# Optimization experiments

Measured on AMD Instinct MI355X. Metric: run time of the kernel, lower is better.

Reference implementation:

```python
import jax, jax.numpy as jnp
import numpy as np

C = 256
CQK = C // 8


def setup_inputs() -> dict:
    key = jax.random.key(0)
    ks = jax.random.split(key, 8)
    B, H, W = 4, 64, 64
    x = jax.random.normal(ks[0], (B, C, H, W), dtype=jnp.float32)
    # 1x1 conv weights are plain [out_c, in_c] matrices + bias
    sq = 1.0 / np.sqrt(C)
    Wq = jax.random.uniform(ks[1], (CQK, C), jnp.float32, -sq, sq)
    bq = jax.random.uniform(ks[2], (CQK,), jnp.float32, -sq, sq)
    Wk = jax.random.uniform(ks[3], (CQK, C), jnp.float32, -sq, sq)
    bk = jax.random.uniform(ks[4], (CQK,), jnp.float32, -sq, sq)
    Wv = jax.random.uniform(ks[5], (C, C), jnp.float32, -sq, sq)
    bv = jax.random.uniform(ks[6], (C,), jnp.float32, -sq, sq)
    gamma = jnp.zeros((1,), dtype=jnp.float32)
    return {"x": x, "Wq": Wq, "bq": bq, "Wk": Wk, "bk": bk, "Wv": Wv, "bv": bv, "gamma": gamma}


def reference(x, Wq, bq, Wk, bk, Wv, bv, gamma):
    B, Cc, H, W = x.shape
    N = H * W
    xf = x.reshape(B, Cc, N)  # [B, C, N]
    # 1x1 convs == channel GEMMs
    q = jnp.einsum('dc,bcn->bdn', Wq, xf) + bq[None, :, None]  # [B, C/8, N]
    k = jnp.einsum('dc,bcn->bdn', Wk, xf) + bk[None, :, None]  # [B, C/8, N]
    v = jnp.einsum('dc,bcn->bdn', Wv, xf) + bv[None, :, None]  # [B, C, N]
    # attention[b, i, j] = softmax_j( q_i . k_j )  (no scaling, as in source)
    attn = jax.nn.softmax(jnp.einsum('bdn,bdm->bnm', q, k), axis=-1)  # [B, N, N]
    # out = value @ attention  (note: NOT attention^T, faithful to source)
    out = jnp.einsum('bcn,bnm->bcm', v, attn)  # [B, C, N]
    out = out.reshape(B, Cc, H, W)
    return gamma[0] * out + x
```

## Files before the change

kernel.cpp:

```cpp
#include <hip/hip_runtime.h>
#include <hip/hip_bf16.h>


#define NB 4
#define CC 256
#define NN 4096
#define L2E 1.44269504088896340f

typedef short  short4v  __attribute__((ext_vector_type(4)));
typedef short  short8v  __attribute__((ext_vector_type(8)));
typedef __bf16 bf16x8   __attribute__((ext_vector_type(8)));
typedef float  f32x4    __attribute__((ext_vector_type(4)));
typedef float  f32x16   __attribute__((ext_vector_type(16)));
typedef unsigned long u64x2 __attribute__((ext_vector_type(2)));
typedef unsigned int u32;

#define AS1 __attribute__((address_space(1)))
#define AS3 __attribute__((address_space(3)))

static __device__ __forceinline__ void gload16(const void* g, void* l) {
  __builtin_amdgcn_global_load_lds((const AS1 u32*)g, (AS3 u32*)l, 16, 0, 0);
}

static __device__ __forceinline__ unsigned short f2bf(float f) {
  union { __bf16 h; unsigned short u; } v; v.h = (__bf16)f; return v.u;
}
static __device__ __forceinline__ float bf2f(unsigned short u) {
  union { unsigned u; float f; } v; v.u = (u32)u << 16; return v.f;
}

union FragU { short8v s; bf16x8 b; unsigned u[4]; };

static __device__ __forceinline__ bf16x8 ld_frag(const unsigned short* p) {
  FragU u; u.s = *(const short8v*)p; return u.b;
}

static __device__ __forceinline__ f32x16 zero16() {
  f32x16 v;
#pragma unroll
  for (int i = 0; i < 16; ++i) v[i] = 0.0f;
  return v;
}

static __device__ __forceinline__ f32x16 mfma32(bf16x8 a, bf16x8 b, f32x16 c) {
  return __builtin_amdgcn_mfma_f32_32x32x16_bf16(a, b, c, 0, 0, 0);
}

__global__ __launch_bounds__(256) void k_wcvt(
    const float* __restrict__ Wq, const float* __restrict__ Wk,
    const float* __restrict__ Wv, unsigned short* __restrict__ Wb)
{
  const int i4 = blockIdx.x * 256 + threadIdx.x;
  const int e = i4 * 4;
  const int row = e >> 8, c = e & 255;
  const float* src = (row < 32) ? (Wq + row * 256 + c)
                   : (row < 64) ? (Wk + (row - 32) * 256 + c)
                                : (Wv + (row - 64) * 256 + c);
  f32x4 v = *(const f32x4*)src;
  short4v s;
#pragma unroll
  for (int j = 0; j < 4; ++j) s[j] = (short)f2bf(v[j]);
  *(short4v*)(Wb + e) = s;
}

__global__ __launch_bounds__(256) void k_proj(
    const float* __restrict__ x, const unsigned short* __restrict__ Wb,
    const float* __restrict__ bq, const float* __restrict__ bk,
    const float* __restrict__ bv,
    unsigned short* __restrict__ Qt, unsigned short* __restrict__ Kt,
    unsigned char* __restrict__ V8)
{
  __shared__ unsigned short xs[32][268];
  const int t = threadIdx.x;
  const int b = blockIdx.y;
  const int n0 = blockIdx.x * 32;
  const int w = t >> 6, l = t & 63, h = l >> 5, col = l & 31;

  const float* xb = x + (size_t)b * CC * NN;
  {
    const int c_off = t >> 3, nl = 4 * (t & 7);
#pragma unroll
    for (int c0 = 0; c0 < CC; c0 += 32) {
      int c = c0 + c_off;
      f32x4 v4 = *(const f32x4*)(xb + (size_t)c * NN + n0 + nl);
#pragma unroll
      for (int j = 0; j < 4; ++j) xs[nl + j][c] = f2bf(v4[j]);
    }
  }
  __syncthreads();

  for (int f = w; f < 10; f += 4) {
    const float* bsrc; int rowbase; int mode; int wrow;
    if (f == 0)      { bsrc = bq; rowbase = 0;            mode = 0; wrow = 0; }
    else if (f == 1) { bsrc = bk; rowbase = 0;            mode = 1; wrow = 32; }
    else             { bsrc = bv; rowbase = (f - 2) * 32; mode = 2; wrow = 64 + rowbase; }

    f32x16 acc0 = zero16();
    const unsigned short* wr = Wb + (size_t)(wrow + col) * 256 + 8 * h;

#pragma unroll
    for (int k0 = 0; k0 < CC; k0 += 16) {
      FragU a;
      a.s = *(const short8v*)(wr + k0);
      const unsigned short* p0 = &xs[col][k0 + 8 * h];
      FragU b0;
      short4v t0a = *(const short4v*)p0, t0b = *(const short4v*)(p0 + 4);
#pragma unroll
      for (int j = 0; j < 4; ++j) { b0.s[j] = t0a[j]; b0.s[4 + j] = t0b[j]; }
      acc0 = mfma32(a.b, b0.b, acc0);
    }

    const int n = n0 + col;
#pragma unroll
    for (int q = 0; q < 4; ++q) {
      f32x4 bias4 = *(const f32x4*)(bsrc + rowbase + 8 * q + 4 * h);
      float vals[4];
#pragma unroll
      for (int i = 0; i < 4; ++i) vals[i] = acc0[4 * q + i] + bias4[i];
      if (mode == 2) {
        const size_t tb = (((size_t)b * (NN >> 4) + (n >> 4)) * 2 + ((n >> 3) & 1)) * CC * 8
                          + (n & 7);
        u32 w01 = __builtin_amdgcn_cvt_pk_fp8_f32(vals[0], vals[1], 0, false);
        u32 w23 = __builtin_amdgcn_cvt_pk_fp8_f32(vals[2], vals[3], 0, false);
        const int cb0 = rowbase + 8 * q + 4 * h;
        V8[tb + (size_t)(cb0 + 0) * 8] = (unsigned char)(w01 & 0xff);
        V8[tb + (size_t)(cb0 + 1) * 8] = (unsigned char)((w01 >> 8) & 0xff);
        V8[tb + (size_t)(cb0 + 2) * 8] = (unsigned char)(w23 & 0xff);
        V8[tb + (size_t)(cb0 + 3) * 8] = (unsigned char)((w23 >> 8) & 0xff);
      } else {
        unsigned short* dst = (mode == 0) ? Qt : Kt;
        const float scale = (mode == 0) ? L2E : 1.0f;
        short4v s4;
#pragma unroll
        for (int i = 0; i < 4; ++i) s4[i] = (short)f2bf(vals[i] * scale);
        *(short4v*)(dst + ((size_t)b * NN + n) * 32 + 8 * q + 4 * h) = s4;
      }
    }
  }
}

__global__ __launch_bounds__(256) void k_rowstats(
    const unsigned short* __restrict__ Qt, const unsigned short* __restrict__ Kt,
    float* __restrict__ cbias)
{
  __shared__ float ssum[4][32];
  const int t = threadIdx.x;
  const int w = t >> 6, l = t & 63, h = l >> 5, col = l & 31;
  const int b = blockIdx.y;
  const int n0 = blockIdx.x * 32;
  const unsigned short* Qb = Qt + (size_t)b * NN * 32;
  const unsigned short* Kb = Kt + (size_t)b * NN * 32;

  bf16x8 bq0 = ld_frag(Qb + (size_t)(n0 + col) * 32 + 8 * h);
  bf16x8 bq1 = ld_frag(Qb + (size_t)(n0 + col) * 32 + 16 + 8 * h);

  float acc = 0.0f;
  const int mbase = w * (NN / 4);
#pragma unroll 2
  for (int mt = 0; mt < 32; ++mt) {
    const int m0 = mbase + mt * 32;
    bf16x8 ak0 = ld_frag(Kb + (size_t)(m0 + col) * 32 + 8 * h);
    bf16x8 ak1 = ld_frag(Kb + (size_t)(m0 + col) * 32 + 16 + 8 * h);
    f32x16 S = zero16();
    S = mfma32(ak0, bq0, S);
    S = mfma32(ak1, bq1, S);
    float p0 = 0.0f, p1 = 0.0f, p2 = 0.0f, p3 = 0.0f;
#pragma unroll
    for (int r = 0; r < 4; ++r) {
      p0 += __builtin_amdgcn_exp2f(S[r]);
      p1 += __builtin_amdgcn_exp2f(S[4 + r]);
      p2 += __builtin_amdgcn_exp2f(S[8 + r]);
      p3 += __builtin_amdgcn_exp2f(S[12 + r]);
    }
    acc += (p0 + p1) + (p2 + p3);
  }
  acc += __shfl_xor(acc, 32);

  if (l < 32) ssum[w][l] = acc;
  __syncthreads();

  if (t < 32) {
    float s = (ssum[0][t] + ssum[1][t]) + (ssum[2][t] + ssum[3][t]);
    cbias[(size_t)b * NN + n0 + t] = -__builtin_amdgcn_logf(s);
  }
}

__global__ __launch_bounds__(512) void k_attn_out(
    const unsigned short* __restrict__ Qt, const unsigned short* __restrict__ Kt,
    const unsigned char* __restrict__ V8,
    const float* __restrict__ cbias,
    unsigned short* __restrict__ pout,
    int nsplit, int nlen)
{
  __shared__ __align__(16) char qbuf[2][2][2048];
  __shared__ __align__(16) char vbuf[3][2][8192];
  __shared__ __align__(16) char ebuf[2][2][4096];

  const int wg = (int)blockIdx.x;
  const int chunk = (int)gridDim.x >> 3;
  const int id2 = (wg & 7) * chunk + (wg >> 3);
  const int per_b = 32 * nsplit;
  const int b = id2 / per_b;
  const int rem = id2 - b * per_b;
  const int ns = rem >> 5;
  const int m0 = (rem & 31) * 128;
  const int nbeg = ns * nlen;

  const int t = threadIdx.x;
  const int w = t >> 6, l = t & 63, h = l >> 5, col = l & 31;
  const int mfp = w & 3;
  const int ccons = (w & 3) * 64;

  const unsigned short* Kb = Kt + (size_t)b * NN * 32;
  const float* cb = cbias + (size_t)b * NN + nbeg;

  bf16x8 bk0 = ld_frag(Kb + (size_t)(m0 + 32 * mfp + col) * 32 + 8 * h);
  bf16x8 bk1 = ld_frag(Kb + (size_t)(m0 + 32 * mfp + col) * 32 + 16 + 8 * h);

  const int ll = l & 15;
  const size_t gqoff = (size_t)(((w & 1) * 16 + ll) * 64 + ((w >> 1) & 1) * 16
                                + (w >> 2) * 32);
  const char* qsrc = (const char*)Qt + ((size_t)b * NN + nbeg) * 64 + gqoff;
  const char* vsrc = (const char*)V8 + ((size_t)b * (NN >> 4) + (nbeg >> 4)) * 4096
                     + (size_t)t * 16;

  f32x16 acc[4][2];
#pragma unroll
  for (int mf = 0; mf < 4; ++mf)
#pragma unroll
    for (int cf = 0; cf < 2; ++cf) acc[mf][cf] = zero16();

  const int J = nlen >> 6;

  if (ll == l) {
    gload16(qsrc, &qbuf[0][0][w * 256]);
    gload16(qsrc + 2048, &qbuf[0][1][w * 256]);
  }
  gload16(vsrc, &vbuf[0][0][w * 1024]);
  gload16(vsrc + 8192, &vbuf[0][1][w * 1024]);
  __syncthreads();

  for (int j = 0; j <= J; ++j) {
    if (j + 1 < J) {
      const size_t qoff = (size_t)(2 * j + 2) * 2048;
      const size_t voff = (size_t)(2 * j + 2) * 8192;
      const int qs = (j + 1) & 1, vs = (j + 1) % 3;
      if (ll == l) {
        gload16(qsrc + qoff, &qbuf[qs][0][w * 256]);
        gload16(qsrc + qoff + 2048, &qbuf[qs][1][w * 256]);
      }
      gload16(vsrc + voff, &vbuf[vs][0][w * 1024]);
      gload16(vsrc + voff + 8192, &vbuf[vs][1][w * 1024]);
    }

    if (w < 4) {
      if (j < J) {
#pragma unroll
        for (int u = 0; u < 2; ++u) {
          const char* qb = &qbuf[j & 1][u][0];
          FragU fq0, fq1;
          fq0.s = *(const short8v*)(qb + l * 16);
          fq1.s = *(const short8v*)(qb + 1024 + l * 16);
          f32x16 S = zero16();
          S = mfma32(fq0.b, bk0, S);
          S = mfma32(fq1.b, bk1, S);

          float e[16];
          const float* cbi = cb + (2 * j + u) * 32;
#pragma unroll
          for (int q = 0; q < 4; ++q) {
            f32x4 cb4 = *(const f32x4*)(cbi + 8 * q + 4 * h);
#pragma unroll
            for (int i = 0; i < 4; ++i)
              e[4 * q + i] = __builtin_amdgcn_exp2f(S[4 * q + i] + cb4[i]);
          }
          u32 wA = __builtin_amdgcn_cvt_pk_fp8_f32(e[0], e[1], 0, false);
          wA = __builtin_amdgcn_cvt_pk_fp8_f32(e[2], e[3], wA, true);
          u32 wB = __builtin_amdgcn_cvt_pk_fp8_f32(e[4], e[5], 0, false);
          wB = __builtin_amdgcn_cvt_pk_fp8_f32(e[6], e[7], wB, true);
          u32 wC = __builtin_amdgcn_cvt_pk_fp8_f32(e[8], e[9], 0, false);
          wC = __builtin_amdgcn_cvt_pk_fp8_f32(e[10], e[11], wC, true);
          u32 wD = __builtin_amdgcn_cvt_pk_fp8_f32(e[12], e[13], 0, false);
          wD = __builtin_amdgcn_cvt_pk_fp8_f32(e[14], e[15], wD, true);
          asm("v_permlane32_swap_b32 %0, %1" : "+v"(wA), "+v"(wB));
          asm("v_permlane32_swap_b32 %0, %1" : "+v"(wC), "+v"(wD));
          u64x2 ev;
          ev[0] = ((unsigned long)wB << 32) | wA;
          ev[1] = ((unsigned long)wD << 32) | wC;
          *(u64x2*)(&ebuf[j & 1][u][mfp * 1024 + l * 16]) = ev;
        }
      }
    } else {
      if (j > 0) {
        const int pv = (j + 2) % 3;
        __builtin_amdgcn_s_setprio(1);
#pragma unroll
        for (int u = 0; u < 2; ++u) {
          const char* vb = &vbuf[pv][u][h * 2048 + (ccons + col) * 8];
          long v00 = *(const long*)(vb);
          long v01 = *(const long*)(vb + 256);
          long v10 = *(const long*)(vb + 4096);
          long v11 = *(const long*)(vb + 4096 + 256);
          const char* eb = &ebuf[(j - 1) & 1][u][l * 16];
          u64x2 ev0 = *(const u64x2*)(eb);
          u64x2 ev1 = *(const u64x2*)(eb + 1024);
          u64x2 ev2 = *(const u64x2*)(eb + 2048);
          u64x2 ev3 = *(const u64x2*)(eb + 3072);
          acc[0][0] = __builtin_amdgcn_mfma_f32_32x32x16_fp8_fp8((long)ev0[0], v00, acc[0][0], 0, 0, 0);
          acc[1][0] = __builtin_amdgcn_mfma_f32_32x32x16_fp8_fp8((long)ev1[0], v00, acc[1][0], 0, 0, 0);
          acc[2][0] = __builtin_amdgcn_mfma_f32_32x32x16_fp8_fp8((long)ev2[0], v00, acc[2][0], 0, 0, 0);
          acc[3][0] = __builtin_amdgcn_mfma_f32_32x32x16_fp8_fp8((long)ev3[0], v00, acc[3][0], 0, 0, 0);
          acc[0][1] = __builtin_amdgcn_mfma_f32_32x32x16_fp8_fp8((long)ev0[0], v01, acc[0][1], 0, 0, 0);
          acc[1][1] = __builtin_amdgcn_mfma_f32_32x32x16_fp8_fp8((long)ev1[0], v01, acc[1][1], 0, 0, 0);
          acc[2][1] = __builtin_amdgcn_mfma_f32_32x32x16_fp8_fp8((long)ev2[0], v01, acc[2][1], 0, 0, 0);
          acc[3][1] = __builtin_amdgcn_mfma_f32_32x32x16_fp8_fp8((long)ev3[0], v01, acc[3][1], 0, 0, 0);
          acc[0][0] = __builtin_amdgcn_mfma_f32_32x32x16_fp8_fp8((long)ev0[1], v10, acc[0][0], 0, 0, 0);
          acc[1][0] = __builtin_amdgcn_mfma_f32_32x32x16_fp8_fp8((long)ev1[1], v10, acc[1][0], 0, 0, 0);
          acc[2][0] = __builtin_amdgcn_mfma_f32_32x32x16_fp8_fp8((long)ev2[1], v10, acc[2][0], 0, 0, 0);
          acc[3][0] = __builtin_amdgcn_mfma_f32_32x32x16_fp8_fp8((long)ev3[1], v10, acc[3][0], 0, 0, 0);
          acc[0][1] = __builtin_amdgcn_mfma_f32_32x32x16_fp8_fp8((long)ev0[1], v11, acc[0][1], 0, 0, 0);
          acc[1][1] = __builtin_amdgcn_mfma_f32_32x32x16_fp8_fp8((long)ev1[1], v11, acc[1][1], 0, 0, 0);
          acc[2][1] = __builtin_amdgcn_mfma_f32_32x32x16_fp8_fp8((long)ev2[1], v11, acc[2][1], 0, 0, 0);
          acc[3][1] = __builtin_amdgcn_mfma_f32_32x32x16_fp8_fp8((long)ev3[1], v11, acc[3][1], 0, 0, 0);
        }
        __builtin_amdgcn_s_setprio(0);
      }
    }

    if (j < J) __syncthreads();
  }

  if (w >= 4) {
    unsigned short* pb = pout + (((size_t)ns * NB + b) * NN + m0) * CC + ccons;
#pragma unroll
    for (int mf = 0; mf < 4; ++mf)
#pragma unroll
      for (int cf = 0; cf < 2; ++cf)
#pragma unroll
        for (int r = 0; r < 16; ++r) {
          int mloc = 32 * mf + (r & 3) + 8 * (r >> 2) + 4 * h;
          pb[(size_t)mloc * CC + 32 * cf + col] = f2bf(acc[mf][cf][r]);
        }
  }
}

__global__ __launch_bounds__(256) void k_comb(
    const unsigned short* __restrict__ pout, const float* __restrict__ x,
    const float* __restrict__ gamma, float* __restrict__ out, int nsplit)
{
  __shared__ float ld[64][65];
  const size_t STRIDE = (size_t)NB * CC * NN;
  const int t = threadIdx.x;
  const int m0 = blockIdx.x * 64, c0 = blockIdx.y * 64, b = blockIdx.z;
  const int ci = t & 63, mo = t >> 6;

  const unsigned short* pb = pout + ((size_t)b * NN + m0) * CC + c0;
#pragma unroll
  for (int rep = 0; rep < 16; ++rep) {
    const int mi = 4 * rep + mo;
    float s = bf2f(pb[(size_t)mi * CC + ci]);
    for (int ns = 1; ns < nsplit; ++ns)
      s += bf2f(pb[ns * STRIDE + (size_t)mi * CC + ci]);
    ld[mi][ci] = s;
  }
  __syncthreads();

  const float g = gamma[0];
  const int mi2 = t & 63;
#pragma unroll
  for (int rep = 0; rep < 16; ++rep) {
    const int cj = 4 * rep + mo;
    const size_t idx = ((size_t)b * CC + c0 + cj) * NN + m0 + mi2;
    out[idx] = g * ld[mi2][cj] + x[idx];
  }
}

extern "C" void kernel_launch(void* const* d_in, const int* in_sizes, int n_in,
                              void* d_out, int out_size, void* d_ws, size_t ws_size,
                              hipStream_t stream) {
  const float* x     = (const float*)d_in[0];
  const float* Wq    = (const float*)d_in[1];
  const float* bq    = (const float*)d_in[2];
  const float* Wk    = (const float*)d_in[3];
  const float* bk    = (const float*)d_in[4];
  const float* Wv    = (const float*)d_in[5];
  const float* bv    = (const float*)d_in[6];
  const float* gamma = (const float*)d_in[7];
  float* out = (float*)d_out;

  char* ws = (char*)d_ws;
  unsigned short* Qt = (unsigned short*)(ws);
  unsigned short* Kt = (unsigned short*)(ws + (1u << 20));
  unsigned char*  V8 = (unsigned char*)(ws + (2u << 20));
  unsigned short* Wb = (unsigned short*)(ws + (6u << 20));
  float* cbias = (float*)(ws + (10u << 20) + (2u << 18));
  const size_t POUT_OFF = (11u << 20);
  unsigned short* pout = (unsigned short*)(ws + POUT_OFF);
  const size_t PART_BYTES = (size_t)NB * CC * NN * 2;

  int nsplit = (ws_size >= POUT_OFF + 2 * PART_BYTES) ? 2 : 1;

  k_wcvt<<<dim3(80), 256, 0, stream>>>(Wq, Wk, Wv, Wb);
  k_proj<<<dim3(NN / 32, NB), 256, 0, stream>>>(x, Wb, bq, bk, bv, Qt, Kt, V8);
  k_rowstats<<<dim3(NN / 32, NB), 256, 0, stream>>>(Qt, Kt, cbias);
  k_attn_out<<<dim3(128 * nsplit), 512, 0, stream>>>(
      Qt, Kt, V8, cbias, pout, nsplit, NN / nsplit);
  k_comb<<<dim3(NN / 64, CC / 64, NB), 256, 0, stream>>>(pout, x, gamma, out, nsplit);
}
```

Measured before the change: 97.12 us.

## Load V directly into registers with new layout; widen rowstats tiles

The V projection output layout is reordered so each PV lane can load its fp8 V fragments with 16-byte global loads straight into registers, dropping the LDS V staging buffer. The main loop is unrolled by two with ping-pong register sets that prefetch the next tile's V while the current one is consumed. Separately, the rowstats kernel now processes 64 query rows per 512-thread block, reusing each K fragment for two MFMA tiles. Risks include higher register pressure in the consumer waves and global-load latency no longer hidden behind LDS.

```diff
diff --git a/kernel.cpp b/kernel.cpp
--- a/kernel.cpp
+++ b/kernel.cpp
@@ -118,15 +118,15 @@
 #pragma unroll
       for (int i = 0; i < 4; ++i) vals[i] = acc0[4 * q + i] + bias4[i];
       if (mode == 2) {
-        const size_t tb = (((size_t)b * (NN >> 4) + (n >> 4)) * 2 + ((n >> 3) & 1)) * CC * 8
-                          + (n & 7);
+        const size_t tb = ((((size_t)b * 128 + (n >> 5)) * 2 + ((n >> 3) & 1)) * 256) * 16
+                          + ((n >> 4) & 1) * 8 + (n & 7);
         u32 w01 = __builtin_amdgcn_cvt_pk_fp8_f32(vals[0], vals[1], 0, false);
         u32 w23 = __builtin_amdgcn_cvt_pk_fp8_f32(vals[2], vals[3], 0, false);
         const int cb0 = rowbase + 8 * q + 4 * h;
-        V8[tb + (size_t)(cb0 + 0) * 8] = (unsigned char)(w01 & 0xff);
-        V8[tb + (size_t)(cb0 + 1) * 8] = (unsigned char)((w01 >> 8) & 0xff);
-        V8[tb + (size_t)(cb0 + 2) * 8] = (unsigned char)(w23 & 0xff);
-        V8[tb + (size_t)(cb0 + 3) * 8] = (unsigned char)((w23 >> 8) & 0xff);
+        V8[tb + (size_t)(cb0 + 0) * 16] = (unsigned char)(w01 & 0xff);
+        V8[tb + (size_t)(cb0 + 1) * 16] = (unsigned char)((w01 >> 8) & 0xff);
+        V8[tb + (size_t)(cb0 + 2) * 16] = (unsigned char)(w23 & 0xff);
+        V8[tb + (size_t)(cb0 + 3) * 16] = (unsigned char)((w23 >> 8) & 0xff);
       } else {
         unsigned short* dst = (mode == 0) ? Qt : Kt;
         const float scale = (mode == 0) ? L2E : 1.0f;
@@ -139,51 +139,154 @@
   }
 }
 
-__global__ __launch_bounds__(256) void k_rowstats(
+__global__ __launch_bounds__(512) void k_rowstats(
     const unsigned short* __restrict__ Qt, const unsigned short* __restrict__ Kt,
     float* __restrict__ cbias)
 {
-  __shared__ float ssum[4][32];
+  __shared__ float ssum[8][64];
   const int t = threadIdx.x;
   const int w = t >> 6, l = t & 63, h = l >> 5, col = l & 31;
   const int b = blockIdx.y;
-  const int n0 = blockIdx.x * 32;
+  const int n0 = blockIdx.x * 64;
   const unsigned short* Qb = Qt + (size_t)b * NN * 32;
   const unsigned short* Kb = Kt + (size_t)b * NN * 32;
 
-  bf16x8 bq0 = ld_frag(Qb + (size_t)(n0 + col) * 32 + 8 * h);
-  bf16x8 bq1 = ld_frag(Qb + (size_t)(n0 + col) * 32 + 16 + 8 * h);
-
-  float acc = 0.0f;
-  const int mbase = w * (NN / 4);
+  bf16x8 bq00 = ld_frag(Qb + (size_t)(n0 + col) * 32 + 8 * h);
+  bf16x8 bq01 = ld_frag(Qb + (size_t)(n0 + col) * 32 + 16 + 8 * h);
+  bf16x8 bq10 = ld_frag(Qb + (size_t)(n0 + 32 + col) * 32 + 8 * h);
+  bf16x8 bq11 = ld_frag(Qb + (size_t)(n0 + 32 + col) * 32 + 16 + 8 * h);
+
+  float acc0 = 0.0f, acc1 = 0.0f;
+  const int mbase = w * (NN / 8);
 #pragma unroll 2
-  for (int mt = 0; mt < 32; ++mt) {
+  for (int mt = 0; mt < 16; ++mt) {
     const int m0 = mbase + mt * 32;
     bf16x8 ak0 = ld_frag(Kb + (size_t)(m0 + col) * 32 + 8 * h);
     bf16x8 ak1 = ld_frag(Kb + (size_t)(m0 + col) * 32 + 16 + 8 * h);
-    f32x16 S = zero16();
-    S = mfma32(ak0, bq0, S);
-    S = mfma32(ak1, bq1, S);
+    f32x16 S0 = zero16(), S1 = zero16();
+    S0 = mfma32(ak0, bq00, S0);
+    S0 = mfma32(ak1, bq01, S0);
+    S1 = mfma32(ak0, bq10, S1);
+    S1 = mfma32(ak1, bq11, S1);
     float p0 = 0.0f, p1 = 0.0f, p2 = 0.0f, p3 = 0.0f;
 #pragma unroll
-    for (int r = 0; r < 4; ++r) {
-      p0 += __builtin_amdgcn_exp2f(S[r]);
-      p1 += __builtin_amdgcn_exp2f(S[4 + r]);
-      p2 += __builtin_amdgcn_exp2f(S[8 + r]);
-      p3 += __builtin_amdgcn_exp2f(S[12 + r]);
+    for (int r = 0; r < 8; ++r) {
+      p0 += __builtin_amdgcn_exp2f(S0[r]);
+      p1 += __builtin_amdgcn_exp2f(S0[8 + r]);
+      p2 += __builtin_amdgcn_exp2f(S1[r]);
+      p3 += __builtin_amdgcn_exp2f(S1[8 + r]);
     }
-    acc += (p0 + p1) + (p2 + p3);
-  }
-  acc += __shfl_xor(acc, 32);
-
-  if (l < 32) ssum[w][l] = acc;
+    acc0 += p0 + p1;
+    acc1 += p2 + p3;
+  }
+  acc0 += __shfl_xor(acc0, 32);
+  acc1 += __shfl_xor(acc1, 32);
+
+  if (l < 32) { ssum[w][l] = acc0; ssum[w][32 + l] = acc1; }
   __syncthreads();
 
-  if (t < 32) {
-    float s = (ssum[0][t] + ssum[1][t]) + (ssum[2][t] + ssum[3][t]);
+  if (t < 64) {
+    float s = 0.0f;
+#pragma unroll
+    for (int wv = 0; wv < 8; ++wv) s += ssum[wv][t];
     cbias[(size_t)b * NN + n0 + t] = -__builtin_amdgcn_logf(s);
   }
 }
+
+#define V_ISSUE(SET, TJ)                                                       \
+  {                                                                            \
+    const char* vg_ = vg + (size_t)(TJ) * 8192;                                \
+    SET##A0 = *(const u64x2*)(vg_);                                            \
+    SET##B0 = *(const u64x2*)(vg_ + 512);                                      \
+    SET##A1 = *(const u64x2*)(vg_ + 8192);                                     \
+    SET##B1 = *(const u64x2*)(vg_ + 8192 + 512);                               \
+  }
+
+#define PV_U(EBP, vA, vB)                                                      \
+  {                                                                            \
+    const char* eb_ = (EBP);                                                   \
+    u64x2 ev0 = *(const u64x2*)(eb_);                                          \
+    u64x2 ev1 = *(const u64x2*)(eb_ + 1024);                                   \
+    u64x2 ev2 = *(const u64x2*)(eb_ + 2048);                                   \
+    u64x2 ev3 = *(const u64x2*)(eb_ + 3072);                                   \
+    long v00 = (long)vA[0], v10 = (long)vA[1];                                 \
+    long v01 = (long)vB[0], v11 = (long)vB[1];                                 \
+    acc[0][0] = __builtin_amdgcn_mfma_f32_32x32x16_fp8_fp8((long)ev0[0], v00, acc[0][0], 0, 0, 0); \
+    acc[1][0] = __builtin_amdgcn_mfma_f32_32x32x16_fp8_fp8((long)ev1[0], v00, acc[1][0], 0, 0, 0); \
+    acc[2][0] = __builtin_amdgcn_mfma_f32_32x32x16_fp8_fp8((long)ev2[0], v00, acc[2][0], 0, 0, 0); \
+    acc[3][0] = __builtin_amdgcn_mfma_f32_32x32x16_fp8_fp8((long)ev3[0], v00, acc[3][0], 0, 0, 0); \
+    acc[0][1] = __builtin_amdgcn_mfma_f32_32x32x16_fp8_fp8((long)ev0[0], v01, acc[0][1], 0, 0, 0); \
+    acc[1][1] = __builtin_amdgcn_mfma_f32_32x32x16_fp8_fp8((long)ev1[0], v01, acc[1][1], 0, 0, 0); \
+    acc[2][1] = __builtin_amdgcn_mfma_f32_32x32x16_fp8_fp8((long)ev2[0], v01, acc[2][1], 0, 0, 0); \
+    acc[3][1] = __builtin_amdgcn_mfma_f32_32x32x16_fp8_fp8((long)ev3[0], v01, acc[3][1], 0, 0, 0); \
+    acc[0][0] = __builtin_amdgcn_mfma_f32_32x32x16_fp8_fp8((long)ev0[1], v10, acc[0][0], 0, 0, 0); \
+    acc[1][0] = __builtin_amdgcn_mfma_f32_32x32x16_fp8_fp8((long)ev1[1], v10, acc[1][0], 0, 0, 0); \
+    acc[2][0] = __builtin_amdgcn_mfma_f32_32x32x16_fp8_fp8((long)ev2[1], v10, acc[2][0], 0, 0, 0); \
+    acc[3][0] = __builtin_amdgcn_mfma_f32_32x32x16_fp8_fp8((long)ev3[1], v10, acc[3][0], 0, 0, 0); \
+    acc[0][1] = __builtin_amdgcn_mfma_f32_32x32x16_fp8_fp8((long)ev0[1], v11, acc[0][1], 0, 0, 0); \
+    acc[1][1] = __builtin_amdgcn_mfma_f32_32x32x16_fp8_fp8((long)ev1[1], v11, acc[1][1], 0, 0, 0); \
+    acc[2][1] = __builtin_amdgcn_mfma_f32_32x32x16_fp8_fp8((long)ev2[1], v11, acc[2][1], 0, 0, 0); \
+    acc[3][1] = __builtin_amdgcn_mfma_f32_32x32x16_fp8_fp8((long)ev3[1], v11, acc[3][1], 0, 0, 0); \
+  }
+
+#define K3_ITER(J, CUR, NXT)                                                   \
+  if ((J) <= KJ) {                                                             \
+    const int j_ = (J);                                                        \
+    if (j_ + 1 < KJ) {                                                         \
+      const size_t qoff_ = (size_t)(2 * j_ + 2) * 2048;                        \
+      const int qs_ = (j_ + 1) & 1;                                            \
+      if (ll == l) {                                                           \
+        gload16(qsrc + qoff_, &qbuf[qs_][0][w * 256]);                         \
+        gload16(qsrc + qoff_ + 2048, &qbuf[qs_][1][w * 256]);                  \
+      }                                                                        \
+    }                                                                          \
+    if (w < 4) {                                                               \
+      if (j_ < KJ) {                                                           \
+        _Pragma("unroll")                                                      \
+        for (int u = 0; u < 2; ++u) {                                          \
+          const char* qb = &qbuf[j_ & 1][u][0];                                \
+          FragU fq0, fq1;                                                      \
+          fq0.s = *(const short8v*)(qb + l * 16);                              \
+          fq1.s = *(const short8v*)(qb + 1024 + l * 16);                       \
+          f32x16 S = zero16();                                                 \
+          S = mfma32(fq0.b, bk0, S);                                           \
+          S = mfma32(fq1.b, bk1, S);                                           \
+          float e[16];                                                         \
+          const float* cbi = cb + (2 * j_ + u) * 32;                           \
+          _Pragma("unroll")                                                    \
+          for (int q = 0; q < 4; ++q) {                                        \
+            f32x4 cb4 = *(const f32x4*)(cbi + 8 * q + 4 * h);                  \
+            _Pragma("unroll")                                                  \
+            for (int i = 0; i < 4; ++i)                                        \
+              e[4 * q + i] = __builtin_amdgcn_exp2f(S[4 * q + i] + cb4[i]);    \
+          }                                                                    \
+          u32 wA = __builtin_amdgcn_cvt_pk_fp8_f32(e[0], e[1], 0, false);      \
+          wA = __builtin_amdgcn_cvt_pk_fp8_f32(e[2], e[3], wA, true);          \
+          u32 wB = __builtin_amdgcn_cvt_pk_fp8_f32(e[4], e[5], 0, false);      \
+          wB = __builtin_amdgcn_cvt_pk_fp8_f32(e[6], e[7], wB, true);          \
+          u32 wC = __builtin_amdgcn_cvt_pk_fp8_f32(e[8], e[9], 0, false);      \
+          wC = __builtin_amdgcn_cvt_pk_fp8_f32(e[10], e[11], wC, true);        \
+          u32 wD = __builtin_amdgcn_cvt_pk_fp8_f32(e[12], e[13], 0, false);    \
+          wD = __builtin_amdgcn_cvt_pk_fp8_f32(e[14], e[15], wD, true);        \
+          asm("v_permlane32_swap_b32 %0, %1" : "+v"(wA), "+v"(wB));            \
+          asm("v_permlane32_swap_b32 %0, %1" : "+v"(wC), "+v"(wD));            \
+          u64x2 ev;                                                            \
+          ev[0] = ((unsigned long)wB << 32) | wA;                              \
+          ev[1] = ((unsigned long)wD << 32) | wC;                              \
+          *(u64x2*)(&ebuf[j_ & 1][u][mfp * 1024 + l * 16]) = ev;               \
+        }                                                                      \
+      }                                                                        \
+    } else {                                                                   \
+      if (j_ < KJ) V_ISSUE(NXT, 2 * j_)                                        \
+      if (j_ > 0) {                                                            \
+        __builtin_amdgcn_s_setprio(1);                                         \
+        PV_U(&ebuf[(j_ - 1) & 1][0][l * 16], CUR##A0, CUR##B0)                 \
+        PV_U(&ebuf[(j_ - 1) & 1][1][l * 16], CUR##A1, CUR##B1)                 \
+        __builtin_amdgcn_s_setprio(0);                                         \
+      }                                                                        \
+    }                                                                          \
+    if (j_ < KJ) __syncthreads();                                              \
+  }
 
 __global__ __launch_bounds__(512) void k_attn_out(
     const unsigned short* __restrict__ Qt, const unsigned short* __restrict__ Kt,
@@ -193,7 +296,6 @@
     int nsplit, int nlen)
 {
   __shared__ __align__(16) char qbuf[2][2][2048];
-  __shared__ __align__(16) char vbuf[3][2][8192];
   __shared__ __align__(16) char ebuf[2][2][4096];
 
   const int wg = (int)blockIdx.x;
@@ -221,8 +323,10 @@
   const size_t gqoff = (size_t)(((w & 1) * 16 + ll) * 64 + ((w >> 1) & 1) * 16
                                 + (w >> 2) * 32);
   const char* qsrc = (const char*)Qt + ((size_t)b * NN + nbeg) * 64 + gqoff;
-  const char* vsrc = (const char*)V8 + ((size_t)b * (NN >> 4) + (nbeg >> 4)) * 4096
-                     + (size_t)t * 16;
+
+  const char* vg = (const char*)V8
+      + (((size_t)b * 128 + (nbeg >> 5)) * 2 + h) * 4096
+      + (size_t)(ccons + col) * 16;
 
   f32x16 acc[4][2];
 #pragma unroll
@@ -230,104 +334,22 @@
 #pragma unroll
     for (int cf = 0; cf < 2; ++cf) acc[mf][cf] = zero16();
 
-  const int J = nlen >> 6;
+  u64x2 S0A0, S0B0, S0A1, S0B1;
+  u64x2 S1A0, S1B0, S1A1, S1B1;
+  S0A0 = S0B0 = S0A1 = S0B1 = (u64x2)0;
+  S1A0 = S1B0 = S1A1 = S1B1 = (u64x2)0;
+
+  const int KJ = nlen >> 6;
 
   if (ll == l) {
     gload16(qsrc, &qbuf[0][0][w * 256]);
     gload16(qsrc + 2048, &qbuf[0][1][w * 256]);
   }
-  gload16(vsrc, &vbuf[0][0][w * 1024]);
-  gload16(vsrc + 8192, &vbuf[0][1][w * 1024]);
   __syncthreads();
 
-  for (int j = 0; j <= J; ++j) {
-    if (j + 1 < J) {
-      const size_t qoff = (size_t)(2 * j + 2) * 2048;
-      const size_t voff = (size_t)(2 * j + 2) * 8192;
-      const int qs = (j + 1) & 1, vs = (j + 1) % 3;
-      if (ll == l) {
-        gload16(qsrc + qoff, &qbuf[qs][0][w * 256]);
-        gload16(qsrc + qoff + 2048, &qbuf[qs][1][w * 256]);
-      }
-      gload16(vsrc + voff, &vbuf[vs][0][w * 1024]);
-      gload16(vsrc + voff + 8192, &vbuf[vs][1][w * 1024]);
-    }
-
-    if (w < 4) {
-      if (j < J) {
-#pragma unroll
-        for (int u = 0; u < 2; ++u) {
-          const char* qb = &qbuf[j & 1][u][0];
-          FragU fq0, fq1;
-          fq0.s = *(const short8v*)(qb + l * 16);
-          fq1.s = *(const short8v*)(qb + 1024 + l * 16);
-          f32x16 S = zero16();
-          S = mfma32(fq0.b, bk0, S);
-          S = mfma32(fq1.b, bk1, S);
-
-          float e[16];
-          const float* cbi = cb + (2 * j + u) * 32;
-#pragma unroll
-          for (int q = 0; q < 4; ++q) {
-            f32x4 cb4 = *(const f32x4*)(cbi + 8 * q + 4 * h);
-#pragma unroll
-            for (int i = 0; i < 4; ++i)
-              e[4 * q + i] = __builtin_amdgcn_exp2f(S[4 * q + i] + cb4[i]);
-          }
-          u32 wA = __builtin_amdgcn_cvt_pk_fp8_f32(e[0], e[1], 0, false);
-          wA = __builtin_amdgcn_cvt_pk_fp8_f32(e[2], e[3], wA, true);
-          u32 wB = __builtin_amdgcn_cvt_pk_fp8_f32(e[4], e[5], 0, false);
-          wB = __builtin_amdgcn_cvt_pk_fp8_f32(e[6], e[7], wB, true);
-          u32 wC = __builtin_amdgcn_cvt_pk_fp8_f32(e[8], e[9], 0, false);
-          wC = __builtin_amdgcn_cvt_pk_fp8_f32(e[10], e[11], wC, true);
-          u32 wD = __builtin_amdgcn_cvt_pk_fp8_f32(e[12], e[13], 0, false);
-          wD = __builtin_amdgcn_cvt_pk_fp8_f32(e[14], e[15], wD, true);
-          asm("v_permlane32_swap_b32 %0, %1" : "+v"(wA), "+v"(wB));
-          asm("v_permlane32_swap_b32 %0, %1" : "+v"(wC), "+v"(wD));
-          u64x2 ev;
-          ev[0] = ((unsigned long)wB << 32) | wA;
-          ev[1] = ((unsigned long)wD << 32) | wC;
-          *(u64x2*)(&ebuf[j & 1][u][mfp * 1024 + l * 16]) = ev;
-        }
-      }
-    } else {
-      if (j > 0) {
-        const int pv = (j + 2) % 3;
-        __builtin_amdgcn_s_setprio(1);
-#pragma unroll
-        for (int u = 0; u < 2; ++u) {
-          const char* vb = &vbuf[pv][u][h * 2048 + (ccons + col) * 8];
-          long v00 = *(const long*)(vb);
-          long v01 = *(const long*)(vb + 256);
-          long v10 = *(const long*)(vb + 4096);
-          long v11 = *(const long*)(vb + 4096 + 256);
-          const char* eb = &ebuf[(j - 1) & 1][u][l * 16];
-          u64x2 ev0 = *(const u64x2*)(eb);
-          u64x2 ev1 = *(const u64x2*)(eb + 1024);
-          u64x2 ev2 = *(const u64x2*)(eb + 2048);
-          u64x2 ev3 = *(const u64x2*)(eb + 3072);
-          acc[0][0] = __builtin_amdgcn_mfma_f32_32x32x16_fp8_fp8((long)ev0[0], v00, acc[0][0], 0, 0, 0);
-          acc[1][0] = __builtin_amdgcn_mfma_f32_32x32x16_fp8_fp8((long)ev1[0], v00, acc[1][0], 0, 0, 0);
-          acc[2][0] = __builtin_amdgcn_mfma_f32_32x32x16_fp8_fp8((long)ev2[0], v00, acc[2][0], 0, 0, 0);
-          acc[3][0] = __builtin_amdgcn_mfma_f32_32x32x16_fp8_fp8((long)ev3[0], v00, acc[3][0], 0, 0, 0);
-          acc[0][1] = __builtin_amdgcn_mfma_f32_32x32x16_fp8_fp8((long)ev0[0], v01, acc[0][1], 0, 0, 0);
-          acc[1][1] = __builtin_amdgcn_mfma_f32_32x32x16_fp8_fp8((long)ev1[0], v01, acc[1][1], 0, 0, 0);
-          acc[2][1] = __builtin_amdgcn_mfma_f32_32x32x16_fp8_fp8((long)ev2[0], v01, acc[2][1], 0, 0, 0);
-          acc[3][1] = __builtin_amdgcn_mfma_f32_32x32x16_fp8_fp8((long)ev3[0], v01, acc[3][1], 0, 0, 0);
-          acc[0][0] = __builtin_amdgcn_mfma_f32_32x32x16_fp8_fp8((long)ev0[1], v10, acc[0][0], 0, 0, 0);
-          acc[1][0] = __builtin_amdgcn_mfma_f32_32x32x16_fp8_fp8((long)ev1[1], v10, acc[1][0], 0, 0, 0);
-          acc[2][0] = __builtin_amdgcn_mfma_f32_32x32x16_fp8_fp8((long)ev2[1], v10, acc[2][0], 0, 0, 0);
-          acc[3][0] = __builtin_amdgcn_mfma_f32_32x32x16_fp8_fp8((long)ev3[1], v10, acc[3][0], 0, 0, 0);
-          acc[0][1] = __builtin_amdgcn_mfma_f32_32x32x16_fp8_fp8((long)ev0[1], v11, acc[0][1], 0, 0, 0);
-          acc[1][1] = __builtin_amdgcn_mfma_f32_32x32x16_fp8_fp8((long)ev1[1], v11, acc[1][1], 0, 0, 0);
-          acc[2][1] = __builtin_amdgcn_mfma_f32_32x32x16_fp8_fp8((long)ev2[1], v11, acc[2][1], 0, 0, 0);
-          acc[3][1] = __builtin_amdgcn_mfma_f32_32x32x16_fp8_fp8((long)ev3[1], v11, acc[3][1], 0, 0, 0);
-        }
-        __builtin_amdgcn_s_setprio(0);
-      }
-    }
-
-    if (j < J) __syncthreads();
+  for (int jj = 0; jj <= KJ; jj += 2) {
+    K3_ITER(jj,     S0, S1)
+    K3_ITER(jj + 1, S1, S0)
   }
 
   if (w >= 4) {
@@ -402,7 +424,7 @@
 
   k_wcvt<<<dim3(80), 256, 0, stream>>>(Wq, Wk, Wv, Wb);
   k_proj<<<dim3(NN / 32, NB), 256, 0, stream>>>(x, Wb, bq, bk, bv, Qt, Kt, V8);
-  k_rowstats<<<dim3(NN / 32, NB), 256, 0, stream>>>(Qt, Kt, cbias);
+  k_rowstats<<<dim3(NN / 64, NB), 512, 0, stream>>>(Qt, Kt, cbias);
   k_attn_out<<<dim3(128 * nsplit), 512, 0, stream>>>(
       Qt, Kt, V8, cbias, pout, nsplit, NN / nsplit);
   k_comb<<<dim3(NN / 64, CC / 64, NB), 256, 0, stream>>>(pout, x, gamma, out, nsplit);
```

New measurement: 94.42 us. 1.03x faster.
